# Kernel optimization log

Hardware: AMD Instinct MI355X
Metric: run time of the kernel (lower is better)

Reference implementation:

```python
import jax, jax.numpy as jnp
import numpy as np


def setup_inputs() -> dict:
    key = jax.random.key(0)
    k1, k2, k3, k4, k5 = jax.random.split(key, 5)
    B, S, N, D = 32, 2048, 16, 128
    H = D // 2
    return {
        "celestial_tensor": jax.random.normal(k1, (B, S, N, D), dtype=jnp.float32),
        "W1": jax.random.normal(k2, (2 * D, H), dtype=jnp.float32) * (1.0 / np.sqrt(2 * D)),
        "b1": jax.random.normal(k3, (H,), dtype=jnp.float32) * 0.01,
        "W2": jax.random.normal(k4, (H, 1), dtype=jnp.float32) * (1.0 / np.sqrt(H)),
        "b2": jax.random.normal(k5, (1,), dtype=jnp.float32) * 0.01,
    }


def reference(celestial_tensor, W1, b1, W2, b2):
    # celestial_tensor: [B, S, N, D]
    mean = celestial_tensor.mean(axis=1)  # [B, N, D] -- dominant memory traffic
    B, N, D = mean.shape
    # Build all ordered pairs (i, j): concat(feat_i, feat_j) -> [B, N, N, 2D]
    fi = jnp.broadcast_to(mean[:, :, None, :], (B, N, N, D))
    fj = jnp.broadcast_to(mean[:, None, :, :], (B, N, N, D))
    edge_in = jnp.concatenate([fi, fj], axis=-1)  # [B, N, N, 2D]
    h = jax.nn.gelu(edge_in @ W1 + b1, approximate=False)  # exact erf GELU (torch default)
    s = jax.nn.sigmoid((h @ W2 + b2)[..., 0])  # [B, N, N]
    # Original fills only i<j with f(feat_i, feat_j) and mirrors it; diagonal stays 0.
    up = jnp.triu(s, k=1)
    return up + jnp.swapaxes(up, -1, -2)
```

## Files before the change

### kernel.cpp

```cpp
#include <hip/hip_runtime.h>
#include <math.h>

#define BB 32
#define SS 2048
#define NN 16
#define DD 128
#define ND (NN * DD)
#define ND4 (ND / 4)
#define HH 64

#define CS 64
#define NCHUNK (SS / CS)

__global__ __launch_bounds__(256) void reduce_mean_kernel(
    const float* __restrict__ x, float* __restrict__ mean) {
  const int blk   = blockIdx.x;
  const int b     = blk >> 5;
  const int chunk = blk & 31;
  const int t     = threadIdx.x;

  const float4* xb = (const float4*)x +
                     (size_t)b * SS * ND4 + (size_t)chunk * CS * ND4;

  const int c0 = t;
  const int c1 = t + 256;

  float4 a0 = make_float4(0.f, 0.f, 0.f, 0.f);
  float4 a1 = make_float4(0.f, 0.f, 0.f, 0.f);

#pragma unroll 4
  for (int s = 0; s < CS; ++s) {
    const float4 v0 = xb[(size_t)s * ND4 + c0];
    const float4 v1 = xb[(size_t)s * ND4 + c1];
    a0.x += v0.x; a0.y += v0.y; a0.z += v0.z; a0.w += v0.w;
    a1.x += v1.x; a1.y += v1.y; a1.z += v1.z; a1.w += v1.w;
  }

  const float inv = 1.0f / (float)SS;
  float* m = mean + (size_t)b * ND;
  atomicAdd(&m[c0 * 4 + 0], a0.x * inv);
  atomicAdd(&m[c0 * 4 + 1], a0.y * inv);
  atomicAdd(&m[c0 * 4 + 2], a0.z * inv);
  atomicAdd(&m[c0 * 4 + 3], a0.w * inv);
  atomicAdd(&m[c1 * 4 + 0], a1.x * inv);
  atomicAdd(&m[c1 * 4 + 1], a1.y * inv);
  atomicAdd(&m[c1 * 4 + 2], a1.z * inv);
  atomicAdd(&m[c1 * 4 + 3], a1.w * inv);
}

__global__ __launch_bounds__(256) void pair_mlp_kernel(
    const float* __restrict__ mean, const float* __restrict__ W1,
    const float* __restrict__ b1, const float* __restrict__ W2,
    const float* __restrict__ b2, float* __restrict__ out) {
  const int wave = (blockIdx.x * 256 + threadIdx.x) >> 6;
  const int lane = threadIdx.x & 63;

  const int b   = wave >> 8;
  const int rem = wave & 255;
  const int i   = rem >> 4;
  const int j   = rem & 15;
  if (i >= j) return;

  const float* mi = mean + (size_t)b * ND + i * DD;
  const float* mj = mean + (size_t)b * ND + j * DD;

  float acc = b1[lane];
#pragma unroll 8
  for (int d = 0; d < DD; ++d) {
    const float wi = W1[d * HH + lane];
    const float wj = W1[(DD + d) * HH + lane];
    acc = fmaf(mi[d], wi, acc);
    acc = fmaf(mj[d], wj, acc);
  }

  const float hk = 0.5f * acc * (1.0f + erff(acc * 0.7071067811865476f));

  float v = hk * W2[lane];
#pragma unroll
  for (int off = 32; off > 0; off >>= 1) v += __shfl_down(v, off, 64);

  if (lane == 0) {
    const float s = 1.0f / (1.0f + expf(-(v + b2[0])));
    out[(size_t)b * NN * NN + i * NN + j] = s;
    out[(size_t)b * NN * NN + j * NN + i] = s;
  }
}

extern "C" void kernel_launch(void* const* d_in, const int* in_sizes, int n_in,
                              void* d_out, int out_size, void* d_ws,
                              size_t ws_size, hipStream_t stream) {
  const float* x  = (const float*)d_in[0];
  const float* W1 = (const float*)d_in[1];
  const float* b1 = (const float*)d_in[2];
  const float* W2 = (const float*)d_in[3];
  const float* b2 = (const float*)d_in[4];
  float* out = (float*)d_out;
  float* mean = (float*)d_ws;

  hipMemsetAsync(mean, 0, (size_t)BB * ND * sizeof(float), stream);

  reduce_mean_kernel<<<BB * NCHUNK, 256, 0, stream>>>(x, mean);

  hipMemsetAsync(out, 0, (size_t)BB * NN * NN * sizeof(float), stream);

  pair_mlp_kernel<<<2048, 256, 0, stream>>>(mean, W1, b1, W2, b2, out);
}
```

Measured before the change: 718.4 us.

## Replace atomic mean reduction with two-pass partials and drop memsets

The atomic-add accumulation of the sequence mean is replaced by a partial-sum kernel that writes per-chunk sums to workspace, followed by a small finalize kernel that sums the chunks and scales. This removes both memsets and the atomic contention. The pair MLP now launches only the 120 upper-triangle pairs per batch instead of masking out idle waves, and it writes the zero diagonal itself. The cost is an extra kernel launch plus a round trip through workspace for the partials. A leftover empty if block remains in the code.

Result: faster. 701.4 us (-2.4%).

```diff
diff --git a/kernel.cpp b/kernel.cpp
--- a/kernel.cpp
+++ b/kernel.cpp
@@ -12,8 +12,10 @@
 #define CS 64
 #define NCHUNK (SS / CS)
 
-__global__ __launch_bounds__(256) void reduce_mean_kernel(
-    const float* __restrict__ x, float* __restrict__ mean) {
+#define PARTIAL_OFF_BYTES (16u * 1024u * 1024u)
+
+__global__ __launch_bounds__(256) void partial_sum_kernel(
+    const float* __restrict__ x, float4* __restrict__ partial) {
   const int blk   = blockIdx.x;
   const int b     = blk >> 5;
   const int chunk = blk & 31;
@@ -36,16 +38,26 @@
     a1.x += v1.x; a1.y += v1.y; a1.z += v1.z; a1.w += v1.w;
   }
 
+  float4* p = partial + (size_t)blk * ND4;
+  p[c0] = a0;
+  p[c1] = a1;
+}
+
+__global__ __launch_bounds__(256) void finalize_mean_kernel(
+    const float4* __restrict__ partial, float4* __restrict__ mean) {
+  const int g = blockIdx.x * 256 + threadIdx.x;
+  const int b = g >> 9;
+  const int c = g & 511;
+
+  float4 a = make_float4(0.f, 0.f, 0.f, 0.f);
+#pragma unroll
+  for (int chunk = 0; chunk < NCHUNK; ++chunk) {
+    const float4 v = partial[((size_t)(b * NCHUNK + chunk)) * ND4 + c];
+    a.x += v.x; a.y += v.y; a.z += v.z; a.w += v.w;
+  }
   const float inv = 1.0f / (float)SS;
-  float* m = mean + (size_t)b * ND;
-  atomicAdd(&m[c0 * 4 + 0], a0.x * inv);
-  atomicAdd(&m[c0 * 4 + 1], a0.y * inv);
-  atomicAdd(&m[c0 * 4 + 2], a0.z * inv);
-  atomicAdd(&m[c0 * 4 + 3], a0.w * inv);
-  atomicAdd(&m[c1 * 4 + 0], a1.x * inv);
-  atomicAdd(&m[c1 * 4 + 1], a1.y * inv);
-  atomicAdd(&m[c1 * 4 + 2], a1.z * inv);
-  atomicAdd(&m[c1 * 4 + 3], a1.w * inv);
+  a.x *= inv; a.y *= inv; a.z *= inv; a.w *= inv;
+  mean[(size_t)b * ND4 + c] = a;
 }
 
 __global__ __launch_bounds__(256) void pair_mlp_kernel(
@@ -55,11 +67,21 @@
   const int wave = (blockIdx.x * 256 + threadIdx.x) >> 6;
   const int lane = threadIdx.x & 63;
 
-  const int b   = wave >> 8;
-  const int rem = wave & 255;
-  const int i   = rem >> 4;
-  const int j   = rem & 15;
-  if (i >= j) return;
+  const int b = wave / 120;
+  int k = wave - b * 120;
+
+  int i = 0;
+#pragma unroll
+  for (int r = 0; r < 15; ++r) {
+    const bool adv = k >= (15 - i);
+    if (adv) { k -= (15 - i); i++; }
+  }
+  const int j = i + 1 + k;
+
+  float* ob = out + (size_t)b * NN * NN;
+  if (wave - b * 120 == 0 && lane < NN) {
+  }
+  const int pk = wave - b * 120;
 
   const float* mi = mean + (size_t)b * ND + i * DD;
   const float* mj = mean + (size_t)b * ND + j * DD;
@@ -81,8 +103,11 @@
 
   if (lane == 0) {
     const float s = 1.0f / (1.0f + expf(-(v + b2[0])));
-    out[(size_t)b * NN * NN + i * NN + j] = s;
-    out[(size_t)b * NN * NN + j * NN + i] = s;
+    ob[i * NN + j] = s;
+    ob[j * NN + i] = s;
+  }
+  if (pk == 0 && lane < NN) {
+    ob[lane * NN + lane] = 0.0f;
   }
 }
 
@@ -95,13 +120,11 @@
   const float* W2 = (const float*)d_in[3];
   const float* b2 = (const float*)d_in[4];
   float* out = (float*)d_out;
-  float* mean = (float*)d_ws;
 
-  hipMemsetAsync(mean, 0, (size_t)BB * ND * sizeof(float), stream);
+  float*  mean    = (float*)d_ws;
+  float4* partial = (float4*)((char*)d_ws + PARTIAL_OFF_BYTES);
 
-  reduce_mean_kernel<<<BB * NCHUNK, 256, 0, stream>>>(x, mean);
-
-  hipMemsetAsync(out, 0, (size_t)BB * NN * NN * sizeof(float), stream);
-
-  pair_mlp_kernel<<<2048, 256, 0, stream>>>(mean, W1, b1, W2, b2, out);
+  partial_sum_kernel<<<BB * NCHUNK, 256, 0, stream>>>(x, partial);
+  finalize_mean_kernel<<<64, 256, 0, stream>>>(partial, (float4*)mean);
+  pair_mlp_kernel<<<960, 256, 0, stream>>>(mean, W1, b1, W2, b2, out);
 }
```
